# Kernel optimization log

Measured on AMD Instinct MI355X. Metric: run time of the kernel, lower is better.

Reference implementation:

```python
import jax, jax.numpy as jnp
import numpy as np

B = 32768          # rays
N = 512            # gaussians
NSH = 4            # -> m = 2*NSH+1 = 9 SH coeffs
H = 512.0
W = 512.0
S_MIN = 1.0 / 30.0       # 1 / n_gaussian_max_pixels
S_MAX = 1.0 / 0.75       # 1 / n_gaussian_min_pixels
MU_BORDER = 1.05
PI_APPROX = 3.1416       # matches the literal in the torch source


def setup_inputs() -> dict:
    key = jax.random.key(0)
    ks = jax.random.split(key, 6)
    # pixel coordinates in [0, W) x [0, H)
    x = jax.random.uniform(ks[0], (B, 2), jnp.float32) * jnp.array([W, H], jnp.float32)
    rgbsh = jax.random.uniform(ks[1], (N, 2 * NSH + 1, 3), jnp.float32)
    opacity = jax.random.uniform(ks[2], (N,), jnp.float32)
    mu = jax.random.uniform(ks[3], (N, 2), jnp.float32) * 2.0 - 1.0
    scale = jax.random.uniform(ks[4], (N, 2), jnp.float32)
    angle = jax.random.uniform(ks[5], (N,), jnp.float32) * 2.0 - 1.0
    return {"x": x, "rgbsh": rgbsh, "opacity": opacity,
            "mu": mu, "scale": scale, "angle": angle}


def _forward(x, rgbsh, opacity, mu, scale, angle):
    wh = jnp.array([W, H], x.dtype)                      # (2,)
    xnorm = x / wh * 2.0 - 1.0                           # (B,2) in [-1,1]
    gmu = jnp.tanh(mu) * MU_BORDER                       # (N,2)
    S = jnp.clip(scale, 0.0, 1.0) * (S_MAX - S_MIN) + S_MIN  # (N,2) inverse radii

    # pixel-space offset ray->gaussian: (x - mu)/2 * (w,h)
    vec = (xnorm[:, None, :] - gmu[None, :, :]) * (wh * 0.5)   # (B,N,2)

    # validity mask (computed under no_grad in torch): |S * vec| < 5
    dist = jnp.linalg.norm(vec * S[None], axis=-1)             # (B,N)
    valid = jax.lax.stop_gradient(dist < 5.0)

    # per-gaussian rotation matrices
    alpha = jnp.tanh(angle) * PI_APPROX                        # (N,)
    c, s = jnp.cos(alpha), jnp.sin(alpha)
    R = jnp.stack([jnp.stack([c, -s], -1),
                   jnp.stack([s,  c], -1)], axis=-2)           # (N,2,2)

    # Mahalanobis-like squared distance: || R @ diag(S) @ vec ||^2
    svec = vec * S[None]                                       # (B,N,2)
    rot = jnp.einsum('nij,bnj->bni', R, svec)                  # (B,N,2)
    d2 = jnp.sum(rot * rot, axis=-1)                           # (B,N)

    # view angle in the gaussian frame
    vnorm = vec / (1e-10 + jnp.linalg.norm(vec, axis=-1, keepdims=True))
    vrot = jnp.einsum('nij,bnj->bni', R, vnorm)                # (B,N,2)
    theta = jnp.arctan2(vrot[..., 0], vrot[..., 1])            # (B,N)

    # 2D SH basis: [1, sin(t), cos(t), sin(2t), cos(2t), ...]
    basis = [jnp.ones_like(theta)]
    for i in range(NSH):
        basis.append(jnp.sin(theta * (i + 1)))
        basis.append(jnp.cos(theta * (i + 1)))
    basis = jnp.stack(basis, axis=-1)                          # (B,N,M)

    rgb = jax.nn.sigmoid(jnp.einsum('bnm,nmc->bnc', basis, rgbsh))  # (B,N,3)
    wgt = jnp.where(valid,
                    jnp.exp(-d2) * jax.nn.sigmoid(opacity)[None, :],
                    jnp.zeros((), x.dtype))                    # (B,N)

    # accumulate_along_rays: per-ray weighted sum over gaussians
    return jnp.einsum('bn,bnc->bc', wgt, rgb)                  # (B,3)


def reference(x, rgbsh, opacity, mu, scale, angle):
    return _forward(x, rgbsh, opacity, mu, scale, angle)
```

## Files before the change

kernel.cpp:

```cpp
#include <hip/hip_runtime.h>

#define BDIM 1024
#define NW   16
#define RPB  64
#define NG   512
#define GPW  (NG / NW)


__global__ void pre_kernel(const float* __restrict__ rgbsh,
                           const float* __restrict__ opacity,
                           const float* __restrict__ mu,
                           const float* __restrict__ scale,
                           const float* __restrict__ angle,
                           float4* __restrict__ wsA,
                           float*  __restrict__ wsH,
                           int N)
{
    int n = blockIdx.x * blockDim.x + threadIdx.x;
    if (n >= N) return;
    const float S_MIN = 1.0f / 30.0f;
    const float S_MAX = 1.0f / 0.75f;
    float gmx = tanhf(mu[2 * n + 0]) * 1.05f;
    float gmy = tanhf(mu[2 * n + 1]) * 1.05f;
    float Sx = fminf(fmaxf(scale[2 * n + 0], 0.0f), 1.0f) * (S_MAX - S_MIN) + S_MIN;
    float Sy = fminf(fmaxf(scale[2 * n + 1], 0.0f), 1.0f) * (S_MAX - S_MIN) + S_MIN;
    float ax = 256.0f * Sx, ay = 256.0f * Sy;
    wsA[n] = make_float4(ax, ay, -gmx * ax, -gmy * ay);
    float a = tanhf(angle[n]) * 3.1416f;
    float sa, ca;
    sincosf(a, &sa, &ca);
    float* hp = wsH + ((size_t)n << 5);
    hp[0] = ca;
    hp[1] = sa;
    hp[2] = 1.0f / (1.0f + expf(-opacity[n]));
    hp[3] = 1.0f / Sx;
    hp[4] = 1.0f / Sy;
    #pragma unroll
    for (int q = 0; q < 27; ++q) hp[5 + q] = rgbsh[n * 27 + q];
}

__global__ __launch_bounds__(BDIM, 8) void splat_kernel(
    const float*  __restrict__ x,
    const float4* __restrict__ wsA,
    const float*  __restrict__ wsH,
    float* __restrict__ out,
    int B)
{
    __shared__ float acc[NW][RPB * 3];
    const int tid  = threadIdx.x;
    const int lane = tid & 63;
    const int w = __builtin_amdgcn_readfirstlane(tid >> 6);

    const int b  = blockIdx.x * RPB + lane;
    const int bb = (b < B) ? b : (B - 1);
    float2 p2 = *(const float2*)(x + 2 * bb);
    float pnx = p2.x * (1.0f / 256.0f) - 1.0f;
    float pny = p2.y * (1.0f / 256.0f) - 1.0f;

    float accR = 0.0f, accG = 0.0f, accB = 0.0f;
    const float4* __restrict__ wA = wsA + w * GPW;
    const float*  __restrict__ wH = wsH + ((size_t)(w * GPW) << 5);

    #pragma unroll 2
    for (int j = 0; j < GPW; ++j) {
        float4 pa = wA[j];
        float sx = fmaf(pnx, pa.x, pa.z);
        float sy = fmaf(pny, pa.y, pa.w);
        float t  = fmaf(sx, sx, sy * sy);
        bool  v  = t < 25.0f;
        if (__any(v)) {
            const float* hp = wH + (j << 5);
            float c   = hp[0], s = hp[1];
            float w0  = hp[2];
            float iSx = hp[3], iSy = hp[4];
            if (v) {
                float rx = fmaf(c, sx, -s * sy);
                float ry = fmaf(s, sx,  c * sy);
                float d2 = fmaf(rx, rx, ry * ry);
                float vx  = sx * iSx;
                float vy  = sy * iSy;
                float len = sqrtf(fmaf(vx, vx, vy * vy));
                float inv = __builtin_amdgcn_rcpf(1e-10f + len);
                float rvx = fmaf(c, vx, -s * vy);
                float rvy = fmaf(s, vx,  c * vy);
                float s1 = rvx * inv, c1 = rvy * inv;
                float s2 = 2.0f * s1 * c1;
                float c2 = fmaf(c1, c1, -s1 * s1);
                float s3 = fmaf(s2, c1,  c2 * s1);
                float c3 = fmaf(c2, c1, -s2 * s1);
                float s4 = 2.0f * s2 * c2;
                float c4 = fmaf(c2, c2, -s2 * s2);
                const float* sh = hp + 5;
                float rr = sh[0], gg = sh[1], bb2 = sh[2];
                rr = fmaf(s1, sh[ 3], rr);  gg = fmaf(s1, sh[ 4], gg);  bb2 = fmaf(s1, sh[ 5], bb2);
                rr = fmaf(c1, sh[ 6], rr);  gg = fmaf(c1, sh[ 7], gg);  bb2 = fmaf(c1, sh[ 8], bb2);
                rr = fmaf(s2, sh[ 9], rr);  gg = fmaf(s2, sh[10], gg);  bb2 = fmaf(s2, sh[11], bb2);
                rr = fmaf(c2, sh[12], rr);  gg = fmaf(c2, sh[13], gg);  bb2 = fmaf(c2, sh[14], bb2);
                rr = fmaf(s3, sh[15], rr);  gg = fmaf(s3, sh[16], gg);  bb2 = fmaf(s3, sh[17], bb2);
                rr = fmaf(c3, sh[18], rr);  gg = fmaf(c3, sh[19], gg);  bb2 = fmaf(c3, sh[20], bb2);
                rr = fmaf(s4, sh[21], rr);  gg = fmaf(s4, sh[22], gg);  bb2 = fmaf(s4, sh[23], bb2);
                rr = fmaf(c4, sh[24], rr);  gg = fmaf(c4, sh[25], gg);  bb2 = fmaf(c4, sh[26], bb2);
                rr  = __builtin_amdgcn_rcpf(1.0f + __expf(-rr));
                gg  = __builtin_amdgcn_rcpf(1.0f + __expf(-gg));
                bb2 = __builtin_amdgcn_rcpf(1.0f + __expf(-bb2));
                float wt = __expf(-d2) * w0;
                accR = fmaf(wt, rr,  accR);
                accG = fmaf(wt, gg,  accG);
                accB = fmaf(wt, bb2, accB);
            }
        }
    }

    acc[w][lane * 3 + 0] = accR;
    acc[w][lane * 3 + 1] = accG;
    acc[w][lane * 3 + 2] = accB;
    __syncthreads();
    if (tid < RPB * 3) {
        float s = 0.0f;
        #pragma unroll
        for (int w2 = 0; w2 < NW; ++w2)
            s += acc[w2][tid];
        const int idx = blockIdx.x * (RPB * 3) + tid;
        if (idx < 3 * B)
            out[idx] = s;
    }
}

extern "C" void kernel_launch(void* const* d_in, const int* in_sizes, int n_in,
                              void* d_out, int out_size, void* d_ws, size_t ws_size,
                              hipStream_t stream) {
    const float* x       = (const float*)d_in[0];
    const float* rgbsh   = (const float*)d_in[1];
    const float* opacity = (const float*)d_in[2];
    const float* mu      = (const float*)d_in[3];
    const float* scale   = (const float*)d_in[4];
    const float* angle   = (const float*)d_in[5];
    float* out = (float*)d_out;

    const int B = in_sizes[0] / 2;
    const int N = in_sizes[2];

    char* ws = (char*)d_ws;
    float4* wsA = (float4*)(ws);
    float*  wsH = (float*)(ws + (size_t)N * 16);

    pre_kernel<<<(N + 255) / 256, 256, 0, stream>>>(rgbsh, opacity, mu, scale,
                                                    angle, wsA, wsH, N);
    splat_kernel<<<(B + RPB - 1) / RPB, BDIM, 0, stream>>>(x, wsA, wsH, out, B);
}
```

Before: 77.29 us.

## Compact valid ray-gaussian pairs into per-wave LDS queue to remove divergence

Instead of running the expensive SH/exp evaluation under a divergent branch where few lanes are active, each wave ballots the validity mask, appends (gaussian, lane) pairs to an LDS queue via prefix popcount, and flushes the queue with all 64 lanes busy. Results go into per-wave shared accumulators with LDS atomics. This targets low SIMD utilisation from sparse validity. In exchange it adds queue writes, LDS atomics, per-item global loads of gaussian params, and a reduction that is now no longer ordered. Because of the atomics, floating-point summation order changes.

```diff
diff --git a/kernel.cpp b/kernel.cpp
--- a/kernel.cpp
+++ b/kernel.cpp
@@ -5,6 +5,7 @@
 #define RPB  64
 #define NG   512
 #define GPW  (NG / NW)
+#define QCAP 256
 
 
 __global__ void pre_kernel(const float* __restrict__ rgbsh,
@@ -47,6 +48,8 @@
     int B)
 {
     __shared__ float acc[NW][RPB * 3];
+    __shared__ float pn[2][RPB];
+    __shared__ unsigned short queue[NW][QCAP];
     const int tid  = threadIdx.x;
     const int lane = tid & 63;
     const int w = __builtin_amdgcn_readfirstlane(tid >> 6);
@@ -57,9 +60,65 @@
     float pnx = p2.x * (1.0f / 256.0f) - 1.0f;
     float pny = p2.y * (1.0f / 256.0f) - 1.0f;
 
-    float accR = 0.0f, accG = 0.0f, accB = 0.0f;
-    const float4* __restrict__ wA = wsA + w * GPW;
-    const float*  __restrict__ wH = wsH + ((size_t)(w * GPW) << 5);
+    if (w == 0) { pn[0][lane] = pnx; pn[1][lane] = pny; }
+    #pragma unroll
+    for (int c = 0; c < 3; ++c) acc[w][lane * 3 + c] = 0.0f;
+    __syncthreads();
+
+    const int g0 = w * GPW;
+    const float4* __restrict__ wA = wsA + g0;
+
+    int qlen = 0;
+
+    auto flush = [&]() {
+        for (int qi = lane; qi < qlen; qi += 64) {
+            const int e  = queue[w][qi];
+            const int l  = e & 63;
+            const int g  = g0 + (e >> 6);
+            const float qx = pn[0][l];
+            const float qy = pn[1][l];
+            const float4 pa = wsA[g];
+            const float sx = fmaf(qx, pa.x, pa.z);
+            const float sy = fmaf(qy, pa.y, pa.w);
+            const float4* hp = (const float4*)(wsH + ((size_t)g << 5));
+            const float4 f0 = hp[0], f1 = hp[1], f2 = hp[2], f3 = hp[3];
+            const float4 f4 = hp[4], f5 = hp[5], f6 = hp[6], f7 = hp[7];
+            const float c = f0.x, s = f0.y, w0 = f0.z, iSx = f0.w, iSy = f1.x;
+            float rx = fmaf(c, sx, -s * sy);
+            float ry = fmaf(s, sx,  c * sy);
+            float d2 = fmaf(rx, rx, ry * ry);
+            float vx  = sx * iSx;
+            float vy  = sy * iSy;
+            float len = sqrtf(fmaf(vx, vx, vy * vy));
+            float inv = __builtin_amdgcn_rcpf(1e-10f + len);
+            float rvx = fmaf(c, vx, -s * vy);
+            float rvy = fmaf(s, vx,  c * vy);
+            float s1 = rvx * inv, c1 = rvy * inv;
+            float s2 = 2.0f * s1 * c1;
+            float c2 = fmaf(c1, c1, -s1 * s1);
+            float s3 = fmaf(s2, c1,  c2 * s1);
+            float c3 = fmaf(c2, c1, -s2 * s1);
+            float s4 = 2.0f * s2 * c2;
+            float c4 = fmaf(c2, c2, -s2 * s2);
+            float rr = f1.y, gg = f1.z, bb2 = f1.w;
+            rr = fmaf(s1, f2.x, rr);  gg = fmaf(s1, f2.y, gg);  bb2 = fmaf(s1, f2.z, bb2);
+            rr = fmaf(c1, f2.w, rr);  gg = fmaf(c1, f3.x, gg);  bb2 = fmaf(c1, f3.y, bb2);
+            rr = fmaf(s2, f3.z, rr);  gg = fmaf(s2, f3.w, gg);  bb2 = fmaf(s2, f4.x, bb2);
+            rr = fmaf(c2, f4.y, rr);  gg = fmaf(c2, f4.z, gg);  bb2 = fmaf(c2, f4.w, bb2);
+            rr = fmaf(s3, f5.x, rr);  gg = fmaf(s3, f5.y, gg);  bb2 = fmaf(s3, f5.z, bb2);
+            rr = fmaf(c3, f5.w, rr);  gg = fmaf(c3, f6.x, gg);  bb2 = fmaf(c3, f6.y, bb2);
+            rr = fmaf(s4, f6.z, rr);  gg = fmaf(s4, f6.w, gg);  bb2 = fmaf(s4, f7.x, bb2);
+            rr = fmaf(c4, f7.y, rr);  gg = fmaf(c4, f7.z, gg);  bb2 = fmaf(c4, f7.w, bb2);
+            rr  = __builtin_amdgcn_rcpf(1.0f + __expf(-rr));
+            gg  = __builtin_amdgcn_rcpf(1.0f + __expf(-gg));
+            bb2 = __builtin_amdgcn_rcpf(1.0f + __expf(-bb2));
+            float wt = __expf(-d2) * w0;
+            atomicAdd(&acc[w][l * 3 + 0], wt * rr);
+            atomicAdd(&acc[w][l * 3 + 1], wt * gg);
+            atomicAdd(&acc[w][l * 3 + 2], wt * bb2);
+        }
+        qlen = 0;
+    };
 
     #pragma unroll 2
     for (int j = 0; j < GPW; ++j) {
@@ -68,52 +127,16 @@
         float sy = fmaf(pny, pa.y, pa.w);
         float t  = fmaf(sx, sx, sy * sy);
         bool  v  = t < 25.0f;
-        if (__any(v)) {
-            const float* hp = wH + (j << 5);
-            float c   = hp[0], s = hp[1];
-            float w0  = hp[2];
-            float iSx = hp[3], iSy = hp[4];
-            if (v) {
-                float rx = fmaf(c, sx, -s * sy);
-                float ry = fmaf(s, sx,  c * sy);
-                float d2 = fmaf(rx, rx, ry * ry);
-                float vx  = sx * iSx;
-                float vy  = sy * iSy;
-                float len = sqrtf(fmaf(vx, vx, vy * vy));
-                float inv = __builtin_amdgcn_rcpf(1e-10f + len);
-                float rvx = fmaf(c, vx, -s * vy);
-                float rvy = fmaf(s, vx,  c * vy);
-                float s1 = rvx * inv, c1 = rvy * inv;
-                float s2 = 2.0f * s1 * c1;
-                float c2 = fmaf(c1, c1, -s1 * s1);
-                float s3 = fmaf(s2, c1,  c2 * s1);
-                float c3 = fmaf(c2, c1, -s2 * s1);
-                float s4 = 2.0f * s2 * c2;
-                float c4 = fmaf(c2, c2, -s2 * s2);
-                const float* sh = hp + 5;
-                float rr = sh[0], gg = sh[1], bb2 = sh[2];
-                rr = fmaf(s1, sh[ 3], rr);  gg = fmaf(s1, sh[ 4], gg);  bb2 = fmaf(s1, sh[ 5], bb2);
-                rr = fmaf(c1, sh[ 6], rr);  gg = fmaf(c1, sh[ 7], gg);  bb2 = fmaf(c1, sh[ 8], bb2);
-                rr = fmaf(s2, sh[ 9], rr);  gg = fmaf(s2, sh[10], gg);  bb2 = fmaf(s2, sh[11], bb2);
-                rr = fmaf(c2, sh[12], rr);  gg = fmaf(c2, sh[13], gg);  bb2 = fmaf(c2, sh[14], bb2);
-                rr = fmaf(s3, sh[15], rr);  gg = fmaf(s3, sh[16], gg);  bb2 = fmaf(s3, sh[17], bb2);
-                rr = fmaf(c3, sh[18], rr);  gg = fmaf(c3, sh[19], gg);  bb2 = fmaf(c3, sh[20], bb2);
-                rr = fmaf(s4, sh[21], rr);  gg = fmaf(s4, sh[22], gg);  bb2 = fmaf(s4, sh[23], bb2);
-                rr = fmaf(c4, sh[24], rr);  gg = fmaf(c4, sh[25], gg);  bb2 = fmaf(c4, sh[26], bb2);
-                rr  = __builtin_amdgcn_rcpf(1.0f + __expf(-rr));
-                gg  = __builtin_amdgcn_rcpf(1.0f + __expf(-gg));
-                bb2 = __builtin_amdgcn_rcpf(1.0f + __expf(-bb2));
-                float wt = __expf(-d2) * w0;
-                accR = fmaf(wt, rr,  accR);
-                accG = fmaf(wt, gg,  accG);
-                accB = fmaf(wt, bb2, accB);
-            }
+        unsigned long long mask = __ballot(v);
+        if (mask) {
+            int prefix = __popcll(mask & ((1ull << lane) - 1ull));
+            if (v) queue[w][qlen + prefix] = (unsigned short)((j << 6) | lane);
+            qlen += __popcll(mask);
+            if (qlen > QCAP - 64) flush();
         }
     }
+    flush();
 
-    acc[w][lane * 3 + 0] = accR;
-    acc[w][lane * 3 + 1] = accG;
-    acc[w][lane * 3 + 2] = accB;
     __syncthreads();
     if (tid < RPB * 3) {
         float s = 0.0f;
```

Result: faster. 72.86 us (-5.7%).
